# Kernel optimization log

Measured on AMD Instinct MI355X. Metric: run time of the kernel, lower is better.

## Reference

```python
import jax, jax.numpy as jnp
import numpy as np

N = 100000   # num_nodes
E = 1600000  # num_edges (avg degree 16)
D = 64       # embed_channels
C = 16       # num_classes
EPSILON = 0.1  # AntiSymmetricConv step size (PyG default)
GAMMA = 0.1    # AntiSymmetricConv diffusion strength (PyG default)


def setup_inputs() -> dict:
    key = jax.random.key(0)
    ks = jax.random.split(key, 9)
    s = 1.0 / np.sqrt(D)
    return {
        "edge_index": jax.random.randint(ks[0], (2, E), 0, N, dtype=jnp.int32),
        "embed_w": jax.random.normal(ks[1], (N, D), dtype=jnp.float32) * 0.1,
        "W_rel": jax.random.normal(ks[2], (D, D), dtype=jnp.float32) * s,   # GraphConv lin_rel weight
        "b_rel": jax.random.normal(ks[3], (D,), dtype=jnp.float32) * s,     # GraphConv lin_rel bias
        "W_root": jax.random.normal(ks[4], (D, D), dtype=jnp.float32) * s,  # GraphConv lin_root weight (no bias)
        "W_anti": jax.random.normal(ks[5], (D, D), dtype=jnp.float32) * s,  # AntiSymmetricConv W
        "b_anti": jax.random.normal(ks[6], (D,), dtype=jnp.float32) * s,    # AntiSymmetricConv bias
        "W_lin": jax.random.normal(ks[7], (C, D), dtype=jnp.float32) * s,   # lin2 weight
        "b_lin": jax.random.normal(ks[8], (C,), dtype=jnp.float32) * s,     # lin2 bias
    }


def reference(edge_index, embed_w, W_rel, b_rel, W_root, W_anti, b_anti, W_lin, b_lin):
    x = embed_w  # [N, D] node features = embedding table
    src, dst = edge_index[0], edge_index[1]
    # phi = GraphConv with 'add' aggregation: lin_rel(sum_j x_j) + lin_root(x)
    agg = jax.ops.segment_sum(x[src], dst, num_segments=N)  # [N, D] sparse gather+scatter-add
    h = agg @ W_rel.T + b_rel + x @ W_root.T
    # antisymmetric weight: W - W^T - gamma * I
    aW = W_anti - W_anti.T - GAMMA * jnp.eye(D, dtype=x.dtype)
    h = x @ aW.T + h + b_anti
    h = jnp.tanh(h)                       # default act of AntiSymmetricConv
    x = x + EPSILON * h                   # single iteration (num_iters=1 default)
    # dropout p=0.0 -> identity
    out = jax.nn.sigmoid(x @ W_lin.T + b_lin)  # [N, C]
    return out
```

## Files before the change

### kernel.cpp

```cpp
#include <hip/hip_runtime.h>
#include <hip/hip_fp16.h>

#define DD 64
#define CC 16
#define EPSILON 0.1f
#define GAMMA 0.1f
#define BSH 6
#define BSZ 64
#define CAP 1280
#define MAXBK 2048
#define PAD 65
#define BCHUNK 8192
#define BTHR 1024

__global__ __launch_bounds__(256) void prep_all(
        const float* __restrict__ x, __half2* __restrict__ xh2,
        int* __restrict__ gcnt,
        const float* __restrict__ Wrel, const float* __restrict__ Wroot,
        const float* __restrict__ Wanti, const float* __restrict__ brel,
        const float* __restrict__ banti,
        float* __restrict__ B_g, float* __restrict__ bc, int N) {
    const int t = threadIdx.x, b = blockIdx.x, G = gridDim.x;
    for (int i = b * 256 + t; i < MAXBK; i += G * 256) gcnt[i] = 0;
    const float2* x2 = (const float2*)x;
    const int M = N * (DD / 2);
    for (int i = b * 256 + t; i < M; i += G * 256) {
        float2 v = x2[i];
        xh2[i] = __float22half2_rn(v);
    }
    if (b == 0) {
        for (int idx = t; idx < 128 * 64; idx += 256) {
            int k = idx >> 6, d = idx & 63;
            float v;
            if (k < 64) {
                v = Wrel[d * 64 + k];
            } else {
                int j = k - 64;
                v = Wroot[d * 64 + j] + Wanti[d * 64 + j] - Wanti[j * 64 + d];
                if (d == j) v -= GAMMA;
            }
            B_g[idx] = v;
        }
        if (t < 64) bc[t] = brel[t] + banti[t];
    }
}

__global__ __launch_bounds__(BTHR) void bin_edges(const int* __restrict__ ei,
                                                  int* __restrict__ gcnt,
                                                  unsigned* __restrict__ binned,
                                                  int E, int NBK) {
    __shared__ int hist[MAXBK];
    __shared__ int hbase[MAXBK];
    const int t = threadIdx.x;
    for (int b = t; b < MAXBK; b += BTHR) hist[b] = 0;
    __syncthreads();
    const int e0 = blockIdx.x * BCHUNK;
    int dsts[BCHUNK / BTHR];
#pragma unroll
    for (int i = 0; i < BCHUNK / BTHR; ++i) {
        int e = e0 + t + BTHR * i;
        dsts[i] = (e < E) ? ei[E + e] : -1;
        if (dsts[i] >= 0) atomicAdd(&hist[dsts[i] >> BSH], 1);
    }
    __syncthreads();
    for (int b = t; b < NBK; b += BTHR) {
        hbase[b] = atomicAdd(&gcnt[b], hist[b]);
        hist[b] = 0;
    }
    __syncthreads();
#pragma unroll
    for (int i = 0; i < BCHUNK / BTHR; ++i) {
        int e = e0 + t + BTHR * i;
        if (dsts[i] >= 0) {
            int src = ei[e], dst = dsts[i];
            int b = dst >> BSH;
            int pos = hbase[b] + atomicAdd(&hist[b], 1);
            if (pos < CAP)
                binned[(size_t)b * CAP + pos] =
                    (unsigned)src | ((unsigned)(dst & (BSZ - 1)) << 17);
        }
    }
}

__global__ __launch_bounds__(512, 8) void mega(
        const float* __restrict__ x, const __half* __restrict__ x_h,
        const int* __restrict__ gcnt, const unsigned* __restrict__ binned,
        const float* __restrict__ B_g, const float* __restrict__ bc,
        const float* __restrict__ Wlin, const float* __restrict__ blin,
        float* __restrict__ out, int N) {
    __shared__ float R0[BSZ * PAD];
    __shared__ float wl_sh[CC * PAD];
    __shared__ int csr[CAP];
    __shared__ int deg[BSZ], offs[BSZ], cur[BSZ];

    const int t = threadIdx.x;
    const int b = blockIdx.x;
    const int nb0 = b << BSH;
    int cnt = gcnt[b];
    if (cnt > CAP) cnt = CAP;
    const unsigned* bl = binned + (size_t)b * CAP;

#pragma unroll
    for (int i = 0; i < 2; ++i) {
        int idx = t + 512 * i;
        wl_sh[(idx >> 6) * PAD + (idx & 63)] = Wlin[idx];
    }
    if (t < BSZ) deg[t] = 0;
    __syncthreads();
    for (int i = t; i < cnt; i += 512) atomicAdd(&deg[bl[i] >> 17], 1);
    __syncthreads();
    if (t < BSZ) offs[t] = deg[t];
    __syncthreads();
    for (int off = 1; off < BSZ; off <<= 1) {
        int v = 0;
        if (t < BSZ && t >= off) v = offs[t - off];
        __syncthreads();
        if (t < BSZ) offs[t] += v;
        __syncthreads();
    }
    if (t < BSZ) {
        int excl = offs[t] - deg[t];
        offs[t] = excl;
        cur[t] = excl;
    }
    __syncthreads();
    for (int i = t; i < cnt; i += 512) {
        unsigned en = bl[i];
        int pos = atomicAdd(&cur[en >> 17], 1);
        csr[pos] = (int)(en & 0x1FFFF);
    }
    __syncthreads();

    {
        const int g = t >> 3, q = t & 7;
        const float4* xh4 = (const float4*)x_h;
        const int i0 = offs[g], dc = deg[g];
        __half2 z = __floats2half2_rn(0.f, 0.f);
        __half2 a0 = z, a1 = z, a2 = z, a3 = z;
        __half2 b0 = z, b1 = z, b2 = z, b3 = z;
        int i = 0;
        for (; i + 1 < dc; i += 2) {
            int s0 = csr[i0 + i], s1 = csr[i0 + i + 1];
            float4 v0 = xh4[s0 * 8 + q];
            float4 v1 = xh4[s1 * 8 + q];
            const __half2* h0 = (const __half2*)&v0;
            const __half2* h1 = (const __half2*)&v1;
            a0 = __hadd2(a0, h0[0]); a1 = __hadd2(a1, h0[1]);
            a2 = __hadd2(a2, h0[2]); a3 = __hadd2(a3, h0[3]);
            b0 = __hadd2(b0, h1[0]); b1 = __hadd2(b1, h1[1]);
            b2 = __hadd2(b2, h1[2]); b3 = __hadd2(b3, h1[3]);
        }
        if (i < dc) {
            int s0 = csr[i0 + i];
            float4 v0 = xh4[s0 * 8 + q];
            const __half2* h0 = (const __half2*)&v0;
            a0 = __hadd2(a0, h0[0]); a1 = __hadd2(a1, h0[1]);
            a2 = __hadd2(a2, h0[2]); a3 = __hadd2(a3, h0[3]);
        }
        float2 f0 = __half22float2(a0) , f1 = __half22float2(a1);
        float2 f2 = __half22float2(a2) , f3 = __half22float2(a3);
        float2 g0 = __half22float2(b0) , g1 = __half22float2(b1);
        float2 g2 = __half22float2(b2) , g3 = __half22float2(b3);
        float* row = &R0[g * PAD + 8 * q];
        row[0] = f0.x + g0.x; row[1] = f0.y + g0.y;
        row[2] = f1.x + g1.x; row[3] = f1.y + g1.y;
        row[4] = f2.x + g2.x; row[5] = f2.y + g2.y;
        row[6] = f3.x + g3.x; row[7] = f3.y + g3.y;
    }
    __syncthreads();

    const int nl = t & 63;
    const int dgw = __builtin_amdgcn_readfirstlane(t >> 6);
    float acc[8];
#pragma unroll
    for (int j = 0; j < 8; ++j) acc[j] = 0.f;
#pragma unroll 8
    for (int k = 0; k < DD; ++k) {
        float a = R0[nl * PAD + k];
        const float* Bk = &B_g[k * DD + dgw * 8];
#pragma unroll
        for (int j = 0; j < 8; ++j) acc[j] = fmaf(a, Bk[j], acc[j]);
    }
    __syncthreads();

    {
        int nn = N - nb0;
        if (nn > BSZ) nn = BSZ;
        const float4* x4 = (const float4*)x;
        for (int idx = t; idx < nn * 16; idx += 512) {
            float4 v = x4[nb0 * 16 + idx];
            float* row = &R0[(idx >> 4) * PAD + (idx & 15) * 4];
            row[0] = v.x; row[1] = v.y; row[2] = v.z; row[3] = v.w;
        }
    }
    __syncthreads();

#pragma unroll 8
    for (int k = 0; k < DD; ++k) {
        float a = R0[nl * PAD + k];
        const float* Bk = &B_g[(DD + k) * DD + dgw * 8];
#pragma unroll
        for (int j = 0; j < 8; ++j) acc[j] = fmaf(a, Bk[j], acc[j]);
    }

#pragma unroll
    for (int j = 0; j < 8; ++j) {
        int d = dgw * 8 + j;
        float h = acc[j] + bc[d];
        float e2 = __expf(2.0f * h);
        float th = 1.0f - 2.0f / (e2 + 1.0f);
        acc[j] = R0[nl * PAD + d] + EPSILON * th;
    }
    __syncthreads();
#pragma unroll
    for (int j = 0; j < 8; ++j) R0[nl * PAD + dgw * 8 + j] = acc[j];
    __syncthreads();

    {
        const int g = t >> 3, q = t & 7;
        const int n = nb0 + g;
        if (n < N) {
            float p0 = blin[2 * q], p1 = blin[2 * q + 1];
#pragma unroll 8
            for (int d = 0; d < DD; ++d) {
                float xv = R0[g * PAD + d];
                p0 = fmaf(xv, wl_sh[(2 * q) * PAD + d], p0);
                p1 = fmaf(xv, wl_sh[(2 * q + 1) * PAD + d], p1);
            }
            float2 o;
            o.x = 1.0f / (1.0f + __expf(-p0));
            o.y = 1.0f / (1.0f + __expf(-p1));
            *(float2*)(out + (size_t)n * CC + 2 * q) = o;
        }
    }
}

extern "C" void kernel_launch(void* const* d_in, const int* in_sizes, int n_in,
                              void* d_out, int out_size, void* d_ws, size_t ws_size,
                              hipStream_t stream) {
    const int*   ei    = (const int*)d_in[0];
    const float* x     = (const float*)d_in[1];
    const float* Wrel  = (const float*)d_in[2];
    const float* brel  = (const float*)d_in[3];
    const float* Wroot = (const float*)d_in[4];
    const float* Wanti = (const float*)d_in[5];
    const float* banti = (const float*)d_in[6];
    const float* Wlin  = (const float*)d_in[7];
    const float* blin  = (const float*)d_in[8];
    float* out = (float*)d_out;

    const int E = in_sizes[0] / 2;
    const int N = in_sizes[1] / DD;
    const int NBK = (N + BSZ - 1) >> BSH;

    __half* x_h = (__half*)d_ws;
    unsigned* binned = (unsigned*)(x_h + (size_t)N * DD);
    int*   gcnt = (int*)(binned + (size_t)MAXBK * CAP);
    float* B_g  = (float*)(gcnt + MAXBK);
    float* bc   = B_g + 128 * 64;

    prep_all<<<512, 256, 0, stream>>>(x, (__half2*)x_h, gcnt, Wrel, Wroot,
                                      Wanti, brel, banti, B_g, bc, N);
    bin_edges<<<(E + BCHUNK - 1) / BCHUNK, BTHR, 0, stream>>>(ei, gcnt, binned, E, NBK);
    mega<<<NBK, 512, 0, stream>>>(x, x_h, gcnt, binned, B_g, bc, Wlin, blin, out, N);
}
```

Baseline: 184.8 us.

## Split edge binning into coarse and fine passes, widen gather unroll

```diff
diff --git a/kernel.cpp b/kernel.cpp
--- a/kernel.cpp
+++ b/kernel.cpp
@@ -10,24 +10,29 @@
 #define CAP 1280
 #define MAXBK 2048
 #define PAD 65
-#define BCHUNK 8192
-#define BTHR 1024
+#define CSH 10
+#define MAXNC 128
+#define CAPC 17408
+#define L1CHUNK 4096
+#define L1THR 512
+#define NSLICE 8
 
 __global__ __launch_bounds__(256) void prep_all(
         const float* __restrict__ x, __half2* __restrict__ xh2,
-        int* __restrict__ gcnt,
+        int* __restrict__ gcntc, int* __restrict__ gcnt,
         const float* __restrict__ Wrel, const float* __restrict__ Wroot,
         const float* __restrict__ Wanti, const float* __restrict__ brel,
         const float* __restrict__ banti,
         float* __restrict__ B_g, float* __restrict__ bc, int N) {
     const int t = threadIdx.x, b = blockIdx.x, G = gridDim.x;
-    for (int i = b * 256 + t; i < MAXBK; i += G * 256) gcnt[i] = 0;
+    for (int i = b * 256 + t; i < MAXNC + MAXBK; i += G * 256) {
+        if (i < MAXNC) gcntc[i] = 0;
+        else gcnt[i - MAXNC] = 0;
+    }
     const float2* x2 = (const float2*)x;
     const int M = N * (DD / 2);
-    for (int i = b * 256 + t; i < M; i += G * 256) {
-        float2 v = x2[i];
-        xh2[i] = __float22half2_rn(v);
-    }
+    for (int i = b * 256 + t; i < M; i += G * 256)
+        xh2[i] = __float22half2_rn(x2[i]);
     if (b == 0) {
         for (int idx = t; idx < 128 * 64; idx += 256) {
             int k = idx >> 6, d = idx & 63;
@@ -45,39 +50,82 @@
     }
 }
 
-__global__ __launch_bounds__(BTHR) void bin_edges(const int* __restrict__ ei,
-                                                  int* __restrict__ gcnt,
-                                                  unsigned* __restrict__ binned,
-                                                  int E, int NBK) {
-    __shared__ int hist[MAXBK];
-    __shared__ int hbase[MAXBK];
+__global__ __launch_bounds__(L1THR) void bin_coarse(const int* __restrict__ ei,
+                                                    int* __restrict__ gcntc,
+                                                    unsigned* __restrict__ binned_c,
+                                                    int E) {
+    __shared__ int hist[MAXNC];
+    __shared__ int hbase[MAXNC];
     const int t = threadIdx.x;
-    for (int b = t; b < MAXBK; b += BTHR) hist[b] = 0;
-    __syncthreads();
-    const int e0 = blockIdx.x * BCHUNK;
-    int dsts[BCHUNK / BTHR];
-#pragma unroll
-    for (int i = 0; i < BCHUNK / BTHR; ++i) {
-        int e = e0 + t + BTHR * i;
+    if (t < MAXNC) hist[t] = 0;
+    __syncthreads();
+    const int e0 = blockIdx.x * L1CHUNK;
+    int dsts[L1CHUNK / L1THR];
+#pragma unroll
+    for (int i = 0; i < L1CHUNK / L1THR; ++i) {
+        int e = e0 + t + L1THR * i;
         dsts[i] = (e < E) ? ei[E + e] : -1;
-        if (dsts[i] >= 0) atomicAdd(&hist[dsts[i] >> BSH], 1);
-    }
-    __syncthreads();
-    for (int b = t; b < NBK; b += BTHR) {
-        hbase[b] = atomicAdd(&gcnt[b], hist[b]);
-        hist[b] = 0;
-    }
-    __syncthreads();
-#pragma unroll
-    for (int i = 0; i < BCHUNK / BTHR; ++i) {
-        int e = e0 + t + BTHR * i;
+        if (dsts[i] >= 0) atomicAdd(&hist[dsts[i] >> CSH], 1);
+    }
+    __syncthreads();
+    if (t < MAXNC) {
+        hbase[t] = hist[t] ? atomicAdd(&gcntc[t], hist[t]) : 0;
+        hist[t] = 0;
+    }
+    __syncthreads();
+#pragma unroll
+    for (int i = 0; i < L1CHUNK / L1THR; ++i) {
         if (dsts[i] >= 0) {
-            int src = ei[e], dst = dsts[i];
-            int b = dst >> BSH;
-            int pos = hbase[b] + atomicAdd(&hist[b], 1);
+            int e = e0 + t + L1THR * i;
+            int src = ei[e];
+            int c = dsts[i] >> CSH;
+            int pos = hbase[c] + atomicAdd(&hist[c], 1);
+            if (pos < CAPC)
+                binned_c[(size_t)c * CAPC + pos] =
+                    (unsigned)src | ((unsigned)(dsts[i] & ((1 << CSH) - 1)) << 17);
+        }
+    }
+}
+
+__global__ __launch_bounds__(256) void bin_fine(const int* __restrict__ gcntc,
+                                                const unsigned* __restrict__ binned_c,
+                                                int* __restrict__ gcnt,
+                                                unsigned* __restrict__ binned) {
+    __shared__ int hist[16];
+    __shared__ int hbase[16];
+    const int t = threadIdx.x;
+    const int c = blockIdx.x >> 3, s = blockIdx.x & (NSLICE - 1);
+    int cnt = gcntc[c];
+    if (cnt > CAPC) cnt = CAPC;
+    const int per = (cnt + NSLICE - 1) / NSLICE;
+    const int i0 = s * per;
+    int i1 = i0 + per;
+    if (i1 > cnt) i1 = cnt;
+    if (t < 16) hist[t] = 0;
+    __syncthreads();
+    const unsigned* bcp = binned_c + (size_t)c * CAPC;
+    unsigned ent[9];
+#pragma unroll
+    for (int j = 0; j < 9; ++j) {
+        int i = i0 + t + j * 256;
+        ent[j] = (i < i1) ? bcp[i] : 0xFFFFFFFFu;
+        if (ent[j] != 0xFFFFFFFFu) atomicAdd(&hist[ent[j] >> (17 + BSH)], 1);
+    }
+    __syncthreads();
+    if (t < 16) {
+        hbase[t] = hist[t] ? atomicAdd(&gcnt[c * 16 + t], hist[t]) : 0;
+        hist[t] = 0;
+    }
+    __syncthreads();
+#pragma unroll
+    for (int j = 0; j < 9; ++j) {
+        if (ent[j] != 0xFFFFFFFFu) {
+            unsigned dstc = ent[j] >> 17;
+            int f = dstc >> BSH;
+            int pos = hbase[f] + atomicAdd(&hist[f], 1);
             if (pos < CAP)
-                binned[(size_t)b * CAP + pos] =
-                    (unsigned)src | ((unsigned)(dst & (BSZ - 1)) << 17);
+                binned[(size_t)(c * 16 + f) * CAP + pos] =
+                    (ent[j] & 0x1FFFF) | ((dstc & (BSZ - 1)) << 17);
         }
     }
 }
@@ -136,36 +184,45 @@
         const float4* xh4 = (const float4*)x_h;
         const int i0 = offs[g], dc = deg[g];
         __half2 z = __floats2half2_rn(0.f, 0.f);
-        __half2 a0 = z, a1 = z, a2 = z, a3 = z;
-        __half2 b0 = z, b1 = z, b2 = z, b3 = z;
+        __half2 A0[4] = {z, z, z, z}, A1[4] = {z, z, z, z};
+        __half2 A2[4] = {z, z, z, z}, A3[4] = {z, z, z, z};
         int i = 0;
-        for (; i + 1 < dc; i += 2) {
+        for (; i + 4 <= dc; i += 4) {
             int s0 = csr[i0 + i], s1 = csr[i0 + i + 1];
+            int s2 = csr[i0 + i + 2], s3 = csr[i0 + i + 3];
             float4 v0 = xh4[s0 * 8 + q];
             float4 v1 = xh4[s1 * 8 + q];
+            float4 v2 = xh4[s2 * 8 + q];
+            float4 v3 = xh4[s3 * 8 + q];
             const __half2* h0 = (const __half2*)&v0;
             const __half2* h1 = (const __half2*)&v1;
-            a0 = __hadd2(a0, h0[0]); a1 = __hadd2(a1, h0[1]);
-            a2 = __hadd2(a2, h0[2]); a3 = __hadd2(a3, h0[3]);
-            b0 = __hadd2(b0, h1[0]); b1 = __hadd2(b1, h1[1]);
-            b2 = __hadd2(b2, h1[2]); b3 = __hadd2(b3, h1[3]);
-        }
-        if (i < dc) {
+            const __half2* h2 = (const __half2*)&v2;
+            const __half2* h3 = (const __half2*)&v3;
+#pragma unroll
+            for (int r = 0; r < 4; ++r) {
+                A0[r] = __hadd2(A0[r], h0[r]);
+                A1[r] = __hadd2(A1[r], h1[r]);
+                A2[r] = __hadd2(A2[r], h2[r]);
+                A3[r] = __hadd2(A3[r], h3[r]);
+            }
+        }
+        for (; i < dc; ++i) {
             int s0 = csr[i0 + i];
             float4 v0 = xh4[s0 * 8 + q];
             const __half2* h0 = (const __half2*)&v0;
-            a0 = __hadd2(a0, h0[0]); a1 = __hadd2(a1, h0[1]);
-            a2 = __hadd2(a2, h0[2]); a3 = __hadd2(a3, h0[3]);
-        }
-        float2 f0 = __half22float2(a0) , f1 = __half22float2(a1);
-        float2 f2 = __half22float2(a2) , f3 = __half22float2(a3);
-        float2 g0 = __half22float2(b0) , g1 = __half22float2(b1);
-        float2 g2 = __half22float2(b2) , g3 = __half22float2(b3);
+#pragma unroll
+            for (int r = 0; r < 4; ++r) A0[r] = __hadd2(A0[r], h0[r]);
+        }
         float* row = &R0[g * PAD + 8 * q];
-        row[0] = f0.x + g0.x; row[1] = f0.y + g0.y;
-        row[2] = f1.x + g1.x; row[3] = f1.y + g1.y;
-        row[4] = f2.x + g2.x; row[5] = f2.y + g2.y;
-        row[6] = f3.x + g3.x; row[7] = f3.y + g3.y;
+#pragma unroll
+        for (int r = 0; r < 4; ++r) {
+            float2 f0 = __half22float2(A0[r]);
+            float2 f1 = __half22float2(A1[r]);
+            float2 f2 = __half22float2(A2[r]);
+            float2 f3 = __half22float2(A3[r]);
+            row[2 * r] = (f0.x + f1.x) + (f2.x + f3.x);
+            row[2 * r + 1] = (f0.y + f1.y) + (f2.y + f3.y);
+        }
     }
     __syncthreads();
 
@@ -252,15 +309,19 @@
     const int E = in_sizes[0] / 2;
     const int N = in_sizes[1] / DD;
     const int NBK = (N + BSZ - 1) >> BSH;
+    const int NC  = (N + (1 << CSH) - 1) >> CSH;
 
     __half* x_h = (__half*)d_ws;
-    unsigned* binned = (unsigned*)(x_h + (size_t)N * DD);
-    int*   gcnt = (int*)(binned + (size_t)MAXBK * CAP);
-    float* B_g  = (float*)(gcnt + MAXBK);
-    float* bc   = B_g + 128 * 64;
-
-    prep_all<<<512, 256, 0, stream>>>(x, (__half2*)x_h, gcnt, Wrel, Wroot,
-                                      Wanti, brel, banti, B_g, bc, N);
-    bin_edges<<<(E + BCHUNK - 1) / BCHUNK, BTHR, 0, stream>>>(ei, gcnt, binned, E, NBK);
+    unsigned* binned_c = (unsigned*)(x_h + (size_t)N * DD);
+    unsigned* binned = binned_c + (size_t)MAXNC * CAPC;
+    int*   gcntc = (int*)(binned + (size_t)MAXBK * CAP);
+    int*   gcnt  = gcntc + MAXNC;
+    float* B_g   = (float*)(gcnt + MAXBK);
+    float* bc    = B_g + 128 * 64;
+
+    prep_all<<<512, 256, 0, stream>>>(x, (__half2*)x_h, gcntc, gcnt, Wrel,
+                                      Wroot, Wanti, brel, banti, B_g, bc, N);
+    bin_coarse<<<(E + L1CHUNK - 1) / L1CHUNK, L1THR, 0, stream>>>(ei, gcntc, binned_c, E);
+    bin_fine<<<NC * NSLICE, 256, 0, stream>>>(gcntc, binned_c, gcnt, binned);
     mega<<<NBK, 512, 0, stream>>>(x, x_h, gcnt, binned, B_g, bc, Wlin, blin, out, N);
 }
```

Result: no change. 184.1 us (-0.4%).
